# Performance work log

Measured on AMD Instinct MI355X. Metric: run time of the kernel, lower is better.

Reference implementation:

```python
import jax, jax.numpy as jnp
import numpy as np

N = 100000       # node_num / batch_node_num
E = 1_600_000    # edges (avg degree 16)
IN_DIM = 256
OUT_DIM = 128
SLOPE = 0.1


def setup_inputs() -> dict:
    key = jax.random.key(0)
    k0, k1, k2, k3, k4 = jax.random.split(key, 5)
    node_feats = jax.random.normal(k0, (N, IN_DIM), jnp.float32)
    W = jax.random.normal(k1, (OUT_DIM, IN_DIM), jnp.float32) * (1.0 / np.sqrt(IN_DIM))
    b = jnp.zeros((OUT_DIM,), jnp.float32)
    # a ~ kaiming_normal for shape [2*out_dim, 1]; stored flat here
    a = jax.random.normal(k2, (2 * OUT_DIM,), jnp.float32) * np.sqrt(2.0 / (2 * OUT_DIM))
    src = jax.random.randint(k3, (E,), 0, N, dtype=jnp.int32)
    dst = jax.random.randint(k4, (E,), 0, N, dtype=jnp.int32)
    return {"node_feats": node_feats, "W": W, "b": b, "a": a, "src": src, "dst": dst}


def reference(node_feats, W, b, a, src, dst):
    n = node_feats.shape[0]
    d = W.shape[0]
    # out_linear_layer
    emb = node_feats @ W.T + b                      # [N, D]
    # append self-loop edges (original_node_edge)
    loop = jnp.arange(n, dtype=src.dtype)
    s = jnp.concatenate([src, loop])                # [E+N]
    t = jnp.concatenate([dst, loop])                # [E+N]
    # concat(emb[s], emb[t]) @ a  ==  emb[s] @ a[:D] + emb[t] @ a[D:]
    logits = emb[s] @ a[:d] + emb[t] @ a[d:]        # [E+N]
    score = jnp.exp(jax.nn.leaky_relu(logits, negative_slope=SLOPE))
    # sparse.mm(matrix, emb) and sparse.mm(matrix, ones): segment sums over src rows
    num = jax.ops.segment_sum(score[:, None] * emb[t], s, num_segments=n)  # [N, D]
    den = jax.ops.segment_sum(score, s, num_segments=n)                    # [N]
    return num / den[:, None]
```

## Files before the change

kernel.cpp:

```cpp
#include <hip/hip_runtime.h>
#include <hip/hip_bf16.h>

#define IN_DIM 256
#define OUT_DIM 128
#define SLOPE 0.1f

typedef __attribute__((ext_vector_type(8))) __bf16 bf16x8;
typedef __attribute__((ext_vector_type(4))) float f32x4;

__global__ void convert_w_kernel(const float* __restrict__ W,
                                 __bf16* __restrict__ Whi,
                                 __bf16* __restrict__ Wlo, int total) {
  int i = blockIdx.x * blockDim.x + threadIdx.x;
  if (i < total) {
    float x = W[i];
    __bf16 h = (__bf16)x;
    __bf16 l = (__bf16)(x - (float)h);
    Whi[i] = h;
    Wlo[i] = l;
  }
}

__global__ __launch_bounds__(256) void gemm_mfma_kernel(
    const float* __restrict__ A,
    const __bf16* __restrict__ Whi,
    const __bf16* __restrict__ Wlo,
    const float* __restrict__ bias,
    const float* __restrict__ avec,
    float* __restrict__ emb,
    float* __restrict__ a1,
    float* __restrict__ a2,
    int N) {
  const int lane = threadIdx.x & 63;
  const int wave = threadIdx.x >> 6;
  const int m0 = blockIdx.x * 64 + wave * 16;
  const int lr = lane & 15;
  const int lg = lane >> 4;

  int arow = m0 + lr;
  if (arow > N - 1) arow = N - 1;
  const float* aptr = A + (size_t)arow * IN_DIM + lg * 8;

  f32x4 acc[8];
#pragma unroll
  for (int t = 0; t < 8; ++t) acc[t] = (f32x4)(0.f);

  for (int k0 = 0; k0 < IN_DIM; k0 += 32) {
    float4 q0 = *(const float4*)(aptr + k0);
    float4 q1 = *(const float4*)(aptr + k0 + 4);
    float qs[8] = {q0.x, q0.y, q0.z, q0.w, q1.x, q1.y, q1.z, q1.w};
    bf16x8 ahi, alo;
#pragma unroll
    for (int j = 0; j < 8; ++j) {
      float x = qs[j];
      __bf16 h = (__bf16)x;
      ahi[j] = h;
      alo[j] = (__bf16)(x - (float)h);
    }
    const int kcol = k0 + lg * 8;
#pragma unroll
    for (int t = 0; t < 8; ++t) {
      const size_t woff = (size_t)(t * 16 + lr) * IN_DIM + kcol;
      bf16x8 bhi = *(const bf16x8*)(Whi + woff);
      bf16x8 blo = *(const bf16x8*)(Wlo + woff);
      acc[t] = __builtin_amdgcn_mfma_f32_16x16x32_bf16(ahi, bhi, acc[t], 0, 0, 0);
      acc[t] = __builtin_amdgcn_mfma_f32_16x16x32_bf16(ahi, blo, acc[t], 0, 0, 0);
      acc[t] = __builtin_amdgcn_mfma_f32_16x16x32_bf16(alo, bhi, acc[t], 0, 0, 0);
    }
  }

  float p1[4] = {0.f, 0.f, 0.f, 0.f};
  float p2[4] = {0.f, 0.f, 0.f, 0.f};
#pragma unroll
  for (int t = 0; t < 8; ++t) {
    const int c = t * 16 + lr;
    const float bv = bias[c];
    const float av1 = avec[c];
    const float av2 = avec[OUT_DIM + c];
#pragma unroll
    for (int v = 0; v < 4; ++v) {
      const int r = m0 + lg * 4 + v;
      const float e = acc[t][v] + bv;
      if (r < N) emb[(size_t)r * OUT_DIM + c] = e;
      p1[v] += e * av1;
      p2[v] += e * av2;
    }
  }
#pragma unroll
  for (int v = 0; v < 4; ++v) {
#pragma unroll
    for (int d = 1; d < 16; d <<= 1) {
      p1[v] += __shfl_xor(p1[v], d, 64);
      p2[v] += __shfl_xor(p2[v], d, 64);
    }
  }
  if (lr == 0) {
#pragma unroll
    for (int v = 0; v < 4; ++v) {
      const int r = m0 + lg * 4 + v;
      if (r < N) { a1[r] = p1[v]; a2[r] = p2[v]; }
    }
  }
}

__global__ void hist_kernel(const int* __restrict__ src, int* __restrict__ deg,
                            int E) {
  int i = blockIdx.x * blockDim.x + threadIdx.x;
  if (i < E) atomicAdd(&deg[src[i]], 1);
}

__global__ __launch_bounds__(1024) void scan1_kernel(
    const int* __restrict__ deg, int* __restrict__ offset,
    int* __restrict__ blocksum, int N) {
  __shared__ int tmp[16];
  const int tid = threadIdx.x;
  const int lane = tid & 63;
  const int wave = tid >> 6;
  int i = blockIdx.x * 1024 + tid;
  int v = (i < N) ? deg[i] : 0;
  int x = v;
#pragma unroll
  for (int d = 1; d < 64; d <<= 1) {
    int y = __shfl_up(x, d, 64);
    if (lane >= d) x += y;
  }
  if (lane == 63) tmp[wave] = x;
  __syncthreads();
  if (tid < 16) {
    int wv = tmp[tid];
#pragma unroll
    for (int d = 1; d < 16; d <<= 1) {
      int y = __shfl_up(wv, d, 16);
      if (tid >= d) wv += y;
    }
    tmp[tid] = wv;
  }
  __syncthreads();
  int waveoff = (wave == 0) ? 0 : tmp[wave - 1];
  if (i < N) offset[i] = waveoff + x - v;
  if (tid == 0) blocksum[blockIdx.x] = tmp[15];
}

__global__ __launch_bounds__(1024) void scan2_kernel(int* __restrict__ blocksum,
                                                     int nb) {
  __shared__ int tmp[16];
  const int tid = threadIdx.x;
  const int lane = tid & 63;
  const int wave = tid >> 6;
  int v = (tid < nb) ? blocksum[tid] : 0;
  int x = v;
#pragma unroll
  for (int d = 1; d < 64; d <<= 1) {
    int y = __shfl_up(x, d, 64);
    if (lane >= d) x += y;
  }
  if (lane == 63) tmp[wave] = x;
  __syncthreads();
  if (tid < 16) {
    int wv = tmp[tid];
#pragma unroll
    for (int d = 1; d < 16; d <<= 1) {
      int y = __shfl_up(wv, d, 16);
      if (tid >= d) wv += y;
    }
    tmp[tid] = wv;
  }
  __syncthreads();
  int waveoff = (wave == 0) ? 0 : tmp[wave - 1];
  if (tid < nb) blocksum[tid] = waveoff + x - v;
}

__global__ void scan3_kernel(int* __restrict__ offset,
                             const int* __restrict__ blocksum,
                             int* __restrict__ pos, int N) {
  int i = blockIdx.x * blockDim.x + threadIdx.x;
  if (i < N) {
    int o = offset[i] + blocksum[i >> 10];
    offset[i] = o;
    pos[i] = o;
  }
}

__global__ void scatter_kernel(const int* __restrict__ src,
                               const int* __restrict__ dst,
                               int* __restrict__ pos,
                               int* __restrict__ tsorted, int E) {
  int i = blockIdx.x * blockDim.x + threadIdx.x;
  if (i < E) {
    int p = atomicAdd(&pos[src[i]], 1);
    tsorted[p] = dst[i];
  }
}

__global__ __launch_bounds__(256) void aggregate_kernel(
    const float* __restrict__ emb, const float* __restrict__ a1,
    const float* __restrict__ a2, const int* __restrict__ offset,
    const int* __restrict__ deg, const int* __restrict__ tsorted,
    float* __restrict__ out, int N) {
  int n = (int)((blockIdx.x * (size_t)blockDim.x + threadIdx.x) >> 6);
  int lane = threadIdx.x & 63;
  if (n >= N) return;
  const int q = lane >> 4;
  const int sub = lane & 15;

  const float as = a1[n];
  const int beg = offset[n];
  const int cnt = deg[n];
  const int items = cnt + 1;
  const int niter = (items + 3) >> 2;

  float4 acc0 = make_float4(0.f, 0.f, 0.f, 0.f);
  float4 acc1 = make_float4(0.f, 0.f, 0.f, 0.f);
  float den = 0.f;

  int idx = q;
  int t = (idx == 0 || idx > cnt) ? n : tsorted[beg + idx - 1];
  float at = a2[t];

  for (int i = 0; i < niter; ++i) {
    const bool valid = (idx < items);
    const float* row = emb + (size_t)t * OUT_DIM + sub * 8;
    const float4 v0 = *(const float4*)row;
    const float4 v1 = *(const float4*)(row + 4);
    const float logit = as + at;
    const int idxn = idx + 4;
    if (i + 1 < niter) {
      int tn = (idxn <= cnt) ? tsorted[beg + idxn - 1] : n;
      t = tn;
      at = a2[tn];
    }
    idx = idxn;
    const float sc = valid ? __expf(logit > 0.f ? logit : SLOPE * logit) : 0.f;
    acc0.x += sc * v0.x; acc0.y += sc * v0.y;
    acc0.z += sc * v0.z; acc0.w += sc * v0.w;
    acc1.x += sc * v1.x; acc1.y += sc * v1.y;
    acc1.z += sc * v1.z; acc1.w += sc * v1.w;
    den += sc;
  }

#pragma unroll
  for (int d = 16; d < 64; d <<= 1) {
    acc0.x += __shfl_xor(acc0.x, d, 64);
    acc0.y += __shfl_xor(acc0.y, d, 64);
    acc0.z += __shfl_xor(acc0.z, d, 64);
    acc0.w += __shfl_xor(acc0.w, d, 64);
    acc1.x += __shfl_xor(acc1.x, d, 64);
    acc1.y += __shfl_xor(acc1.y, d, 64);
    acc1.z += __shfl_xor(acc1.z, d, 64);
    acc1.w += __shfl_xor(acc1.w, d, 64);
    den    += __shfl_xor(den,    d, 64);
  }

  if (q == 0) {
    const float inv = 1.0f / den;
    float* op = out + (size_t)n * OUT_DIM + sub * 8;
    *(float4*)op = make_float4(acc0.x * inv, acc0.y * inv, acc0.z * inv,
                               acc0.w * inv);
    *(float4*)(op + 4) = make_float4(acc1.x * inv, acc1.y * inv, acc1.z * inv,
                                     acc1.w * inv);
  }
}

extern "C" void kernel_launch(void* const* d_in, const int* in_sizes, int n_in,
                              void* d_out, int out_size, void* d_ws,
                              size_t ws_size, hipStream_t stream) {
  const float* node_feats = (const float*)d_in[0];
  const float* W = (const float*)d_in[1];
  const float* bias = (const float*)d_in[2];
  const float* avec = (const float*)d_in[3];
  const int* src = (const int*)d_in[4];
  const int* dst = (const int*)d_in[5];
  float* out = (float*)d_out;

  const int OUT = in_sizes[2];
  const int IN = in_sizes[1] / OUT;
  const int N = in_sizes[0] / IN;
  const int E = in_sizes[4];
  const int NB = (N + 1023) / 1024;
  const int WTOT = in_sizes[1];

  char* p = (char*)d_ws;
  auto alloc = [&](size_t bytes) {
    void* r = (void*)p;
    p += (bytes + 255) & ~(size_t)255;
    return r;
  };
  float* emb = (float*)alloc((size_t)N * OUT * sizeof(float));
  float* a1 = (float*)alloc((size_t)N * sizeof(float));
  float* a2 = (float*)alloc((size_t)N * sizeof(float));
  int* deg = (int*)alloc((size_t)N * sizeof(int));
  int* offset = (int*)alloc((size_t)N * sizeof(int));
  int* pos = (int*)alloc((size_t)N * sizeof(int));
  int* blocksum = (int*)alloc((size_t)NB * sizeof(int));
  int* tsorted = (int*)alloc((size_t)E * sizeof(int));
  __bf16* Whi = (__bf16*)alloc((size_t)WTOT * sizeof(__bf16));
  __bf16* Wlo = (__bf16*)alloc((size_t)WTOT * sizeof(__bf16));

  hipMemsetAsync(deg, 0, (size_t)N * sizeof(int), stream);

  convert_w_kernel<<<(WTOT + 255) / 256, 256, 0, stream>>>(W, Whi, Wlo, WTOT);
  hist_kernel<<<(E + 255) / 256, 256, 0, stream>>>(src, deg, E);

  gemm_mfma_kernel<<<(N + 63) / 64, 256, 0, stream>>>(
      node_feats, Whi, Wlo, bias, avec, emb, a1, a2, N);

  scan1_kernel<<<NB, 1024, 0, stream>>>(deg, offset, blocksum, N);
  scan2_kernel<<<1, 1024, 0, stream>>>(blocksum, NB);
  scan3_kernel<<<(N + 255) / 256, 256, 0, stream>>>(offset, blocksum, pos, N);

  scatter_kernel<<<(E + 255) / 256, 256, 0, stream>>>(src, dst, pos, tsorted,
                                                      E);

  aggregate_kernel<<<(N + 3) / 4, 256, 0, stream>>>(emb, a1, a2, offset, deg,
                                                    tsorted, out, N);
}
```

Baseline: 580.5 us.

## Switch GEMM to fp16 split-A with W staged in swizzled LDS

Replaces the three-pass bf16 hi/lo split GEMM with a two-pass fp16 scheme. The activation is still split into hi and lo halves, but W is kept as a single fp16 copy, which drops one MFMA per tile and the Wlo buffer. Each block now stages the whole fp16 W matrix (64 KB) into LDS with an XOR swizzle, so the inner loop reads W from LDS instead of global memory. The fp16 range and rounding of W change accuracy slightly, and 64 KB of LDS per block may limit how many blocks fit on a CU.

```diff
diff --git a/kernel.cpp b/kernel.cpp
--- a/kernel.cpp
+++ b/kernel.cpp
@@ -5,67 +5,77 @@
 #define OUT_DIM 128
 #define SLOPE 0.1f
 
-typedef __attribute__((ext_vector_type(8))) __bf16 bf16x8;
+typedef __attribute__((ext_vector_type(8))) _Float16 f16x8;
 typedef __attribute__((ext_vector_type(4))) float f32x4;
+typedef __attribute__((ext_vector_type(8))) unsigned short u16x8;
 
 __global__ void convert_w_kernel(const float* __restrict__ W,
-                                 __bf16* __restrict__ Whi,
-                                 __bf16* __restrict__ Wlo, int total) {
+                                 _Float16* __restrict__ Wf, int total) {
   int i = blockIdx.x * blockDim.x + threadIdx.x;
-  if (i < total) {
-    float x = W[i];
-    __bf16 h = (__bf16)x;
-    __bf16 l = (__bf16)(x - (float)h);
-    Whi[i] = h;
-    Wlo[i] = l;
-  }
+  if (i < total) Wf[i] = (_Float16)W[i];
 }
 
 __global__ __launch_bounds__(256) void gemm_mfma_kernel(
     const float* __restrict__ A,
-    const __bf16* __restrict__ Whi,
-    const __bf16* __restrict__ Wlo,
+    const _Float16* __restrict__ Wf,
     const float* __restrict__ bias,
     const float* __restrict__ avec,
     float* __restrict__ emb,
     float* __restrict__ a1,
     float* __restrict__ a2,
     int N) {
-  const int lane = threadIdx.x & 63;
-  const int wave = threadIdx.x >> 6;
+  __shared__ _Float16 wlds[32768];
+
+  const int tid = threadIdx.x;
+
+#pragma unroll
+  for (int i = 0; i < 16; ++i) {
+    int chunk = tid + i * 256;
+    int f = chunk << 4;
+    int n = f >> 9;
+    int o = f & 511;
+    int osrc = o ^ ((n & 7) << 4);
+    u16x8 v = *(const u16x8*)((const char*)Wf + (size_t)n * 512 + osrc);
+    *(u16x8*)((char*)wlds + f) = v;
+  }
+  __syncthreads();
+
+  const int lane = tid & 63;
+  const int wave = tid >> 6;
   const int m0 = blockIdx.x * 64 + wave * 16;
   const int lr = lane & 15;
-  const int lg = lane >> 4;
+  const int kg = lane >> 4;
 
   int arow = m0 + lr;
   if (arow > N - 1) arow = N - 1;
-  const float* aptr = A + (size_t)arow * IN_DIM + lg * 8;
+  const float* aptr = A + (size_t)arow * IN_DIM + kg * 8;
 
   f32x4 acc[8];
 #pragma unroll
   for (int t = 0; t < 8; ++t) acc[t] = (f32x4)(0.f);
+
+  const int rowbase = lr * 512;
+  const int swzmask = (lr & 7) << 4;
 
   for (int k0 = 0; k0 < IN_DIM; k0 += 32) {
     float4 q0 = *(const float4*)(aptr + k0);
     float4 q1 = *(const float4*)(aptr + k0 + 4);
     float qs[8] = {q0.x, q0.y, q0.z, q0.w, q1.x, q1.y, q1.z, q1.w};
-    bf16x8 ahi, alo;
+    f16x8 ahi, alo;
 #pragma unroll
     for (int j = 0; j < 8; ++j) {
       float x = qs[j];
-      __bf16 h = (__bf16)x;
+      _Float16 h = (_Float16)x;
       ahi[j] = h;
-      alo[j] = (__bf16)(x - (float)h);
-    }
-    const int kcol = k0 + lg * 8;
+      alo[j] = (_Float16)(x - (float)h);
+    }
+    const int ko = ((k0 * 2 + kg * 16) ^ swzmask);
+    const char* wl = (const char*)wlds + rowbase + ko;
 #pragma unroll
     for (int t = 0; t < 8; ++t) {
-      const size_t woff = (size_t)(t * 16 + lr) * IN_DIM + kcol;
-      bf16x8 bhi = *(const bf16x8*)(Whi + woff);
-      bf16x8 blo = *(const bf16x8*)(Wlo + woff);
-      acc[t] = __builtin_amdgcn_mfma_f32_16x16x32_bf16(ahi, bhi, acc[t], 0, 0, 0);
-      acc[t] = __builtin_amdgcn_mfma_f32_16x16x32_bf16(ahi, blo, acc[t], 0, 0, 0);
-      acc[t] = __builtin_amdgcn_mfma_f32_16x16x32_bf16(alo, bhi, acc[t], 0, 0, 0);
+      f16x8 bf = *(const f16x8*)(wl + t * 8192);
+      acc[t] = __builtin_amdgcn_mfma_f32_16x16x32_f16(ahi, bf, acc[t], 0, 0, 0);
+      acc[t] = __builtin_amdgcn_mfma_f32_16x16x32_f16(alo, bf, acc[t], 0, 0, 0);
     }
   }
 
@@ -79,7 +89,7 @@
     const float av2 = avec[OUT_DIM + c];
 #pragma unroll
     for (int v = 0; v < 4; ++v) {
-      const int r = m0 + lg * 4 + v;
+      const int r = m0 + kg * 4 + v;
       const float e = acc[t][v] + bv;
       if (r < N) emb[(size_t)r * OUT_DIM + c] = e;
       p1[v] += e * av1;
@@ -97,7 +107,7 @@
   if (lr == 0) {
 #pragma unroll
     for (int v = 0; v < 4; ++v) {
-      const int r = m0 + lg * 4 + v;
+      const int r = m0 + kg * 4 + v;
       if (r < N) { a1[r] = p1[v]; a2[r] = p2[v]; }
     }
   }
@@ -293,16 +303,15 @@
   int* pos = (int*)alloc((size_t)N * sizeof(int));
   int* blocksum = (int*)alloc((size_t)NB * sizeof(int));
   int* tsorted = (int*)alloc((size_t)E * sizeof(int));
-  __bf16* Whi = (__bf16*)alloc((size_t)WTOT * sizeof(__bf16));
-  __bf16* Wlo = (__bf16*)alloc((size_t)WTOT * sizeof(__bf16));
+  _Float16* Wfp = (_Float16*)alloc((size_t)WTOT * sizeof(_Float16));
 
   hipMemsetAsync(deg, 0, (size_t)N * sizeof(int), stream);
 
-  convert_w_kernel<<<(WTOT + 255) / 256, 256, 0, stream>>>(W, Whi, Wlo, WTOT);
+  convert_w_kernel<<<(WTOT + 255) / 256, 256, 0, stream>>>(W, Wfp, WTOT);
   hist_kernel<<<(E + 255) / 256, 256, 0, stream>>>(src, deg, E);
 
   gemm_mfma_kernel<<<(N + 63) / 64, 256, 0, stream>>>(
-      node_feats, Whi, Wlo, bias, avec, emb, a1, a2, N);
+      node_feats, Wfp, bias, avec, emb, a1, a2, N);
 
   scan1_kernel<<<NB, 1024, 0, stream>>>(deg, offset, blocksum, N);
   scan2_kernel<<<1, 1024, 0, stream>>>(blocksum, NB);
```

Result: faster. 515.8 us (-11.1%).
